# Optimization experiments

Measured on AMD Instinct MI355X. Metric: run time of the kernel, lower is better.

Reference implementation:

```python
import jax, jax.numpy as jnp
import numpy as np

NHEAD = 8
NPTS = 4
LN_EPS = 1e-5


def pos_embed(H, W, nf):
    # create_pos_embedding with normalize=True, temperature=10000, scale=2*pi
    scale = 2.0 * np.pi
    eps = 1e-6
    y_e = jnp.arange(1, H + 1, dtype=jnp.float32)
    y_e = y_e / (y_e[-1] + eps) * scale
    x_e = jnp.arange(1, W + 1, dtype=jnp.float32)
    x_e = x_e / (x_e[-1] + eps) * scale
    i = jnp.arange(nf, dtype=jnp.float32)
    dim_t = 10000.0 ** (2.0 * jnp.floor(i / 2.0) / nf)
    def enc(e):
        p = e[:, None] / dim_t  # [len, nf]
        return jnp.stack([jnp.sin(p[:, 0::2]), jnp.cos(p[:, 1::2])], axis=-1).reshape(e.shape[0], -1)
    py = enc(y_e)  # [H, nf]
    px = enc(x_e)  # [W, nf]
    pos = jnp.concatenate([
        jnp.broadcast_to(py[:, None, :], (H, W, nf)),
        jnp.broadcast_to(px[None, :, :], (H, W, nf)),
    ], axis=-1)  # [H, W, 2*nf], channel order (pos_y, pos_x) as in torch cat
    return pos.reshape(H * W, 2 * nf)


def layernorm(x, s, b):
    m = x.mean(-1, keepdims=True)
    v = x.var(-1, keepdims=True)
    return (x - m) * jax.lax.rsqrt(v + LN_EPS) * s + b


def bilinear_sample(value, loc, H, W):
    # value [B, HW, Hd, dh]; loc [B, Q, Hd, P, 2] normalized to [0,1] (x, y)
    # Matches F.grid_sample(align_corners=False, padding_mode='zeros') with grid = 2*loc - 1
    B, HW, Hd, dh = value.shape
    Q = loc.shape[1]
    v = value.transpose(0, 2, 1, 3)  # [B, Hd, HW, dh]
    x = loc[..., 0] * W - 0.5
    y = loc[..., 1] * H - 0.5
    x0 = jnp.floor(x)
    y0 = jnp.floor(y)
    wx1 = x - x0
    wy1 = y - y0
    x0i = x0.astype(jnp.int32)
    y0i = y0.astype(jnp.int32)
    def t(a):  # [B, Q, Hd, P] -> [B, Hd, Q*P]
        return a.transpose(0, 2, 1, 3).reshape(B, Hd, -1)
    def gather(xi, yi):
        valid = ((xi >= 0) & (xi < W) & (yi >= 0) & (yi < H)).astype(v.dtype)
        idx = jnp.clip(yi, 0, H - 1) * W + jnp.clip(xi, 0, W - 1)
        g = jnp.take_along_axis(v, t(idx)[..., None], axis=2)  # [B, Hd, Q*P, dh]
        return g * t(valid)[..., None]
    g00 = gather(x0i, y0i)
    g10 = gather(x0i + 1, y0i)
    g01 = gather(x0i, y0i + 1)
    g11 = gather(x0i + 1, y0i + 1)
    out = (g00 * t((1 - wx1) * (1 - wy1))[..., None]
           + g10 * t(wx1 * (1 - wy1))[..., None]
           + g01 * t((1 - wx1) * wy1)[..., None]
           + g11 * t(wx1 * wy1)[..., None])
    return out.reshape(B, Hd, Q, NPTS, dh)


def _forward(x, merge_w, merge_b, off_w, off_b, aw_w, aw_b, val_w, val_b, out_w, out_b,
             n1_s, n1_b, l1_w, l1_b, l2_w, l2_b, n2_s, n2_b, outc_w, outc_b):
    B, N, C, H, W = x.shape
    D = merge_w.shape[0]
    dh = D // NHEAD
    Q = H * W
    # merge: 1x1 conv + relu
    src = jax.nn.relu(jnp.einsum('bchw,dc->bhwd', x.reshape(B, N * C, H, W), merge_w) + merge_b)
    src = src.reshape(B, Q, D)
    pos = pos_embed(H, W, D // 2)[None].astype(x.dtype)  # [1, Q, D]
    # reference points (valid_ratios = 1): centers of cells, normalized
    ys = (jnp.arange(H, dtype=x.dtype) + 0.5) / H
    xs = (jnp.arange(W, dtype=x.dtype) + 0.5) / W
    gx, gy = jnp.meshgrid(xs, ys, indexing='xy')  # each [H, W]
    ref = jnp.stack([gx, gy], axis=-1).reshape(1, Q, 2)
    norm = jnp.array([W, H], dtype=x.dtype)  # offset normalizer (W, H) for (x, y)
    n_layers = off_w.shape[0]
    for l in range(n_layers):
        q = src + pos
        off = (q @ off_w[l] + off_b[l]).reshape(B, Q, NHEAD, NPTS, 2)
        aw = jax.nn.softmax((q @ aw_w[l] + aw_b[l]).reshape(B, Q, NHEAD, NPTS), axis=-1)
        val = (src @ val_w[l] + val_b[l]).reshape(B, Q, NHEAD, dh)
        loc = ref[:, :, None, None, :] + off / norm  # [B, Q, Hd, P, 2]
        samp = bilinear_sample(val, loc, H, W)  # [B, Hd, Q, P, dh]
        o = (samp * aw.transpose(0, 2, 1, 3)[..., None]).sum(3)  # [B, Hd, Q, dh]
        o = o.transpose(0, 2, 1, 3).reshape(B, Q, D) @ out_w[l] + out_b[l]
        src = layernorm(src + o, n1_s[l], n1_b[l])
        ff = jax.nn.relu(src @ l1_w[l] + l1_b[l]) @ l2_w[l] + l2_b[l]
        src = layernorm(src + ff, n2_s[l], n2_b[l])
    feat = src.reshape(B, H, W, D)
    out = jax.nn.relu(jnp.einsum('bhwc,dc->bhwd', feat, outc_w) + outc_b)
    return out.transpose(0, 3, 1, 2)  # [B, D, H, W]


def setup_inputs() -> dict:
    key = jax.random.key(0)
    B, N, Cb, H, W = 1, 4, 128, 120, 360
    D, Dff, L = 128, 512, 3
    ks = jax.random.split(key, 12)
    def rn(k, shape, s=0.02):
        return jax.random.normal(k, shape, dtype=jnp.float32) * s
    return {
        'x': jax.random.normal(ks[0], (B, N, Cb, H, W), dtype=jnp.float32),
        'merge_w': rn(ks[1], (D, N * Cb)),
        'merge_b': jnp.zeros((D,), jnp.float32),
        'off_w': rn(ks[2], (L, D, NHEAD * NPTS * 2)),
        'off_b': rn(ks[3], (L, NHEAD * NPTS * 2), 0.5),
        'aw_w': rn(ks[4], (L, D, NHEAD * NPTS)),
        'aw_b': jnp.zeros((L, NHEAD * NPTS), jnp.float32),
        'val_w': rn(ks[5], (L, D, D)),
        'val_b': jnp.zeros((L, D), jnp.float32),
        'out_w': rn(ks[6], (L, D, D)),
        'out_b': jnp.zeros((L, D), jnp.float32),
        'n1_s': jnp.ones((L, D), jnp.float32),
        'n1_b': jnp.zeros((L, D), jnp.float32),
        'l1_w': rn(ks[7], (L, D, Dff)),
        'l1_b': jnp.zeros((L, Dff), jnp.float32),
        'l2_w': rn(ks[8], (L, Dff, D)),
        'l2_b': jnp.zeros((L, D), jnp.float32),
        'n2_s': jnp.ones((L, D), jnp.float32),
        'n2_b': jnp.zeros((L, D), jnp.float32),
        'outc_w': rn(ks[9], (D, D)),
        'outc_b': jnp.zeros((D,), jnp.float32),
    }


def reference(x, merge_w, merge_b, off_w, off_b, aw_w, aw_b, val_w, val_b, out_w, out_b,
              n1_s, n1_b, l1_w, l1_b, l2_w, l2_b, n2_s, n2_b, outc_w, outc_b):
    return _forward(x, merge_w, merge_b, off_w, off_b, aw_w, aw_b, val_w, val_b, out_w, out_b,
                    n1_s, n1_b, l1_w, l1_b, l2_w, l2_b, n2_s, n2_b, outc_w, outc_b)
```

## Files before the change

### kernel.cpp

```cpp
#include <hip/hip_runtime.h>
#include <hip/hip_bf16.h>
#include <math.h>

#define Q_TOT 43200
#define H_ 120
#define W_ 360

typedef unsigned short ushort_t;
typedef float f32x4 __attribute__((ext_vector_type(4)));
typedef float f32x2 __attribute__((ext_vector_type(2)));
typedef unsigned short u16x4 __attribute__((ext_vector_type(4)));
typedef unsigned short u16x8 __attribute__((ext_vector_type(8)));
using short8 = __attribute__((ext_vector_type(8))) short;

static __device__ __forceinline__ float b2f(unsigned short u){
  return __uint_as_float(((unsigned)u) << 16);
}
static __device__ __forceinline__ unsigned short f2b(float f){
  unsigned u = __float_as_uint(f);
  unsigned r = (u + 0x7fffu + ((u >> 16) & 1u)) >> 16;
  return (unsigned short)r;
}

#define SWZ(row, byte) ((byte) ^ (((row) & 7) << 4))
#define SWZ3(row, byte) ((byte) ^ ((((row) ^ ((row) >> 3)) & 7) << 4))

#define CVT_TOT 615072
__global__ __launch_bounds__(256) void cvt_kernel(
    const float* p0, const float* p1, const float* p2, const float* p3,
    const float* p4, const float* p5, const float* p6, const float* p7,
    const float* p8, const float* p9, const float* p10, const float* p11,
    const float* p12, const float* p13, const float* p14, const float* p15,
    const float* p16, const float* p17, const float* p18, const float* p19,
    ushort_t* __restrict__ dst){
  const float* ps[20] = {p0,p1,p2,p3,p4,p5,p6,p7,p8,p9,p10,p11,p12,p13,p14,p15,p16,p17,p18,p19};
  const int offs[20] = {0,65536,65664,90240,90432,102720,102816,151968,152352,201504,
                        201888,202272,202656,399264,400800,597408,597792,598176,598560,614944};
  int gid = blockIdx.x*256 + threadIdx.x;
  if (gid >= CVT_TOT) return;
  int s = 0;
  #pragma unroll
  for (int i=1;i<20;i++) s += (gid >= offs[i]) ? 1 : 0;
  dst[gid] = f2b(ps[s][gid - offs[s]]);
}

#define CVTT_TOT 528384
__global__ __launch_bounds__(256) void cvtT_kernel(
    const float* __restrict__ vw, const float* __restrict__ ow,
    const float* __restrict__ w1, const float* __restrict__ w2,
    const float* __restrict__ offw, const float* __restrict__ aww,
    ushort_t* __restrict__ dst){
  int gid = blockIdx.x*256 + threadIdx.x;
  if (gid >= CVTT_TOT) return;
  if (gid >= 491520){
    int e = gid - 491520;
    int l = e / 12288, rem = e - l*12288;
    int n = rem >> 7, k = rem & 127;
    float v = (n < 64) ? offw[((size_t)l*128 + k)*64 + n]
                       : aww [((size_t)l*128 + k)*32 + (n-64)];
    dst[gid] = f2b(v);
    return;
  }
  const float* s; int K, N, off;
  if (gid < 49152)      { s = vw; K = 128; N = 128; off = 0; }
  else if (gid < 98304) { s = ow; K = 128; N = 128; off = 49152; }
  else if (gid < 294912){ s = w1; K = 128; N = 512; off = 98304; }
  else                  { s = w2; K = 512; N = 128; off = 294912; }
  int e = gid - off;
  int per = K*N;
  int l = e / per, rem = e - l*per;
  int n = rem / K, k = rem - n*K;
  dst[gid] = f2b(s[(size_t)l*per + (size_t)k*N + n]);
}

__global__ __launch_bounds__(256) void postab_kernel(float* __restrict__ tab){
  int gid = blockIdx.x*256 + threadIdx.x;
  if (gid >= 480*64) return;
  int row = gid >> 6, k = gid & 63;
  int m = k >> 1;
  float t = powf(10000.0f, (float)m * (1.0f/32.0f));
  float e;
  if (row < 120) e = (float)(row+1)   * (6.283185307179586f/((float)H_+1e-6f));
  else           e = (float)(row-119) * (6.283185307179586f/((float)W_+1e-6f));
  float p = e / t;
  tab[gid] = (k & 1) ? cosf(p) : sinf(p);
}

__global__ __launch_bounds__(256) void merge_mfma(const float* __restrict__ x,
    const ushort_t* __restrict__ mw,
    const ushort_t* __restrict__ mb,
    float* __restrict__ src){
  __shared__ ushort_t xt[2][64*128];
  const int tid = threadIdx.x;
  const int wave = tid >> 6, lane = tid & 63;
  const int lr = lane & 15, kg = lane >> 4;
  const int q0 = blockIdx.x * 64;
  const int qq4 = (tid & 15) * 4;
  const int c8  = (tid >> 4) * 8;
  const int qrow = wave*16 + lr;

  f32x4 v[8];
  #pragma unroll
  for (int cc=0;cc<8;cc++)
    v[cc] = *(const f32x4*)(x + (size_t)(c8 + cc)*Q_TOT + q0 + qq4);
  #pragma unroll
  for (int qq=0;qq<4;qq++){
    int row = qq4 + qq;
    u16x8 pk;
    #pragma unroll
    for (int cc=0;cc<8;cc++) pk[cc] = f2b(v[cc][qq]);
    *(u16x8*)((char*)xt[0] + SWZ3(row, row*256 + c8*2)) = pk;
  }
  __syncthreads();

  f32x4 acc[8];
  #pragma unroll
  for (int dt=0; dt<8; dt++) acc[dt] = (f32x4){0.f,0.f,0.f,0.f};

  for (int ch = 0; ch < 4; ch++){
    f32x4 v2[8];
    if (ch < 3){
      #pragma unroll
      for (int cc=0;cc<8;cc++)
        v2[cc] = *(const f32x4*)(x + (size_t)((ch+1)*128 + c8 + cc)*Q_TOT + q0 + qq4);
    }
    const ushort_t* xb = xt[ch & 1];
    short8 xfc[4];
    #pragma unroll
    for (int ks=0; ks<4; ks++)
      xfc[ks] = *(const short8*)((const char*)xb + SWZ3(qrow, qrow*256 + (ks*32 + kg*8)*2));
    short8 wfr[2][4];
    #pragma unroll
    for (int ks=0; ks<4; ks++)
      wfr[0][ks] = *(const short8*)(mw + (size_t)(lr)*512 + ch*128 + ks*32 + kg*8);
    #pragma unroll
    for (int dt=0; dt<8; dt++){
      if (dt < 7){
        const int nr = (dt+1)*16 + lr;
        #pragma unroll
        for (int ks=0; ks<4; ks++)
          wfr[(dt+1)&1][ks] = *(const short8*)(mw + (size_t)nr*512 + ch*128 + ks*32 + kg*8);
      }
      #pragma unroll
      for (int ks=0; ks<4; ks++)
        acc[dt] = __builtin_amdgcn_mfma_f32_16x16x32_bf16(xfc[ks], wfr[dt&1][ks], acc[dt], 0, 0, 0);
    }
    if (ch < 3){
      ushort_t* xn = xt[(ch+1) & 1];
      #pragma unroll
      for (int qq=0;qq<4;qq++){
        int row = qq4 + qq;
        u16x8 pk;
        #pragma unroll
        for (int cc=0;cc<8;cc++) pk[cc] = f2b(v2[cc][qq]);
        *(u16x8*)((char*)xn + SWZ3(row, row*256 + c8*2)) = pk;
      }
      __syncthreads();
    }
  }
  #pragma unroll
  for (int dt=0; dt<8; dt++){
    float bb = b2f(mb[dt*16 + lr]);
    #pragma unroll
    for (int r=0; r<4; r++){
      int q = q0 + wave*16 + kg*4 + r;
      float vv = acc[dt][r] + bb;
      src[(size_t)q*128 + dt*16 + lr] = vv > 0.f ? vv : 0.f;
    }
  }
}

__global__ __launch_bounds__(256) void qv_mfma(const float* __restrict__ src,
    const float* __restrict__ py, const float* __restrict__ px,
    const ushort_t* __restrict__ owt,
    const ushort_t* __restrict__ ob, const ushort_t* __restrict__ awb,
    const ushort_t* __restrict__ vwt,
    const ushort_t* __restrict__ vb,
    float* __restrict__ loc, float* __restrict__ awg,
    ushort_t* __restrict__ valbf){
  __shared__ ushort_t a_lds[64*128];
  __shared__ ushort_t qlds[64*128];
  const int tid = threadIdx.x;
  const int wave = tid >> 6, lane = tid & 63;
  const int lr = lane & 15, kg = lane >> 4;
  const int q0 = blockIdx.x * 64;
  short8 yf[2][4];
  #pragma unroll
  for (int ks=0; ks<4; ks++)
    yf[0][ks] = *(const short8*)(vwt + (size_t)lr*128 + ks*32 + kg*8);
  {
    int row = tid >> 2, c0 = (tid & 3) * 32;
    int q = q0 + row, qy = q / W_, qx = q - qy*W_;
    const float* sp = src + (size_t)q*128 + c0;
    const float* tp = (c0 < 64) ? (py + qy*64 + c0) : (px + qx*64 + (c0 - 64));
    #pragma unroll
    for (int i=0;i<4;i++){
      f32x4 s0 = *(const f32x4*)(sp + i*8), s1 = *(const f32x4*)(sp + i*8 + 4);
      f32x4 t0 = *(const f32x4*)(tp + i*8), t1 = *(const f32x4*)(tp + i*8 + 4);
      u16x8 pa, pq;
      #pragma unroll
      for (int j=0;j<4;j++){
        pa[j] = f2b(s0[j]);        pa[4+j] = f2b(s1[j]);
        pq[j] = f2b(s0[j]+t0[j]);  pq[4+j] = f2b(s1[j]+t1[j]);
      }
      int byte = row*256 + (c0 + i*8)*2;
      *(u16x8*)((char*)a_lds + SWZ(row, byte)) = pa;
      *(u16x8*)((char*)qlds + SWZ(row, byte)) = pq;
    }
  }
  __syncthreads();
  const int qrow = wave*16 + lr;
  short8 xf[4], xq[4];
  #pragma unroll
  for (int ks=0; ks<4; ks++){
    xf[ks] = *(const short8*)((const char*)a_lds + SWZ(qrow, qrow*256 + (ks*32 + kg*8)*2));
    xq[ks] = *(const short8*)((const char*)qlds + SWZ(qrow, qrow*256 + (ks*32 + kg*8)*2));
  }
  f32x4 va[8];
  #pragma unroll
  for (int dt=0; dt<8; dt++) va[dt] = (f32x4){0.f,0.f,0.f,0.f};
  #pragma unroll
  for (int dt=0; dt<8; dt++){
    if (dt < 7){
      const int nr = (dt+1)*16 + lr;
      #pragma unroll
      for (int ks=0; ks<4; ks++)
        yf[(dt+1)&1][ks] = *(const short8*)(vwt + (size_t)nr*128 + ks*32 + kg*8);
    }
    #pragma unroll
    for (int ks=0; ks<4; ks++)
      va[dt] = __builtin_amdgcn_mfma_f32_16x16x32_bf16(xf[ks], yf[dt&1][ks], va[dt], 0, 0, 0);
  }
  f32x4 qa[6];
  #pragma unroll
  for (int nt=0; nt<6; nt++) qa[nt] = (f32x4){0.f,0.f,0.f,0.f};
  short8 of[2][4];
  #pragma unroll
  for (int ks=0; ks<4; ks++)
    of[0][ks] = *(const short8*)(owt + (size_t)lr*128 + ks*32 + kg*8);
  #pragma unroll
  for (int nt=0; nt<6; nt++){
    if (nt < 5){
      const int nr = (nt+1)*16 + lr;
      #pragma unroll
      for (int ks=0; ks<4; ks++)
        of[(nt+1)&1][ks] = *(const short8*)(owt + (size_t)nr*128 + ks*32 + kg*8);
    }
    #pragma unroll
    for (int ks=0; ks<4; ks++)
      qa[nt] = __builtin_amdgcn_mfma_f32_16x16x32_bf16(xq[ks], of[nt&1][ks], qa[nt], 0, 0, 0);
  }
  #pragma unroll
  for (int dt=0; dt<8; dt++){
    float bb = b2f(vb[dt*16 + lr]);
    #pragma unroll
    for (int r=0; r<4; r++){
      int q = q0 + wave*16 + kg*4 + r;
      valbf[(size_t)q*128 + dt*16 + lr] = f2b(va[dt][r] + bb);
    }
  }
  #pragma unroll
  for (int r=0; r<4; r++){
    int q = q0 + wave*16 + kg*4 + r;
    int qy = q / W_, qx = q - qy*W_;
    float qxf = (float)qx, qyf = (float)qy;
    #pragma unroll
    for (int dt=0; dt<4; dt++){
      int n = dt*16 + lr;
      float v = qa[dt][r] + b2f(ob[n]);
      loc[(size_t)q*64 + n] = ((n & 1) ? qyf : qxf) + v;
    }
    #pragma unroll
    for (int d4=0; d4<2; d4++){
      int idx = d4*16 + lr;
      float v = qa[4+d4][r] + b2f(awb[idx]);
      float mx = fmaxf(v, __shfl_xor(v, 1, 64));
      mx = fmaxf(mx, __shfl_xor(mx, 2, 64));
      float e = expf(v - mx);
      float s = e + __shfl_xor(e, 1, 64);
      s = s + __shfl_xor(s, 2, 64);
      awg[(size_t)q*32 + idx] = e / s;
    }
  }
}

__global__ __launch_bounds__(256) void outln_mfma(const float* __restrict__ A,
    const ushort_t* __restrict__ wt,
    const ushort_t* __restrict__ bias,
    const ushort_t* __restrict__ gs, const ushort_t* __restrict__ gb,
    float* srcio){
  __shared__ ushort_t a_lds[64*128];
  const int tid = threadIdx.x;
  const int wave = tid >> 6, lane = tid & 63;
  const int lr = lane & 15, kg = lane >> 4;
  const int q0 = blockIdx.x * 64;
  short8 yf[2][4];
  #pragma unroll
  for (int ks=0; ks<4; ks++)
    yf[0][ks] = *(const short8*)(wt + (size_t)lr*128 + ks*32 + kg*8);
  {
    int row = tid >> 2, c0 = (tid & 3) * 32;
    const float* sp = A + (size_t)(q0+row)*128 + c0;
    #pragma unroll
    for (int i=0;i<4;i++){
      f32x4 v0 = *(const f32x4*)(sp + i*8);
      f32x4 v1 = *(const f32x4*)(sp + i*8 + 4);
      u16x8 pk;
      #pragma unroll
      for (int j=0;j<4;j++){ pk[j]=f2b(v0[j]); pk[4+j]=f2b(v1[j]); }
      int byte = row*256 + (c0 + i*8)*2;
      *(u16x8*)((char*)a_lds + SWZ(row, byte)) = pk;
    }
  }
  __syncthreads();
  const int qrow = wave*16 + lr;
  short8 xf[4];
  #pragma unroll
  for (int ks=0; ks<4; ks++)
    xf[ks] = *(const short8*)((const char*)a_lds + SWZ(qrow, qrow*256 + (ks*32 + kg*8)*2));
  f32x4 acc[8];
  #pragma unroll
  for (int dt=0; dt<8; dt++) acc[dt] = (f32x4){0.f,0.f,0.f,0.f};
  #pragma unroll
  for (int dt=0; dt<8; dt++){
    if (dt < 7){
      const int nr = (dt+1)*16 + lr;
      #pragma unroll
      for (int ks=0; ks<4; ks++)
        yf[(dt+1)&1][ks] = *(const short8*)(wt + (size_t)nr*128 + ks*32 + kg*8);
    }
    #pragma unroll
    for (int ks=0; ks<4; ks++)
      acc[dt] = __builtin_amdgcn_mfma_f32_16x16x32_bf16(xf[ks], yf[dt&1][ks], acc[dt], 0, 0, 0);
  }
  float g4[8], be4[8], bi4[8];
  #pragma unroll
  for (int dt=0; dt<8; dt++){
    g4[dt] = b2f(gs[dt*16+lr]); be4[dt] = b2f(gb[dt*16+lr]); bi4[dt] = b2f(bias[dt*16+lr]);
  }
  #pragma unroll
  for (int r=0; r<4; r++){
    const int q = q0 + wave*16 + kg*4 + r;
    float vals[8];
    float s1 = 0.f, s2 = 0.f;
    #pragma unroll
    for (int dt=0; dt<8; dt++){
      float v = acc[dt][r] + bi4[dt] + srcio[(size_t)q*128 + dt*16 + lr];
      vals[dt] = v; s1 += v; s2 += v*v;
    }
    #pragma unroll
    for (int m=1; m<16; m<<=1){ s1 += __shfl_xor(s1, m, 64); s2 += __shfl_xor(s2, m, 64); }
    float mean = s1*(1.f/128.f);
    float var  = s2*(1.f/128.f) - mean*mean;
    float inv  = rsqrtf(var + 1e-5f);
    #pragma unroll
    for (int dt=0; dt<8; dt++)
      srcio[(size_t)q*128 + dt*16 + lr] = (vals[dt]-mean)*inv*g4[dt] + be4[dt];
  }
}

__global__ __launch_bounds__(512, 4) void ffn_mfma(
    const ushort_t* __restrict__ w1t,
    const ushort_t* __restrict__ b1,
    const ushort_t* __restrict__ w2t,
    const ushort_t* __restrict__ b2,
    const ushort_t* __restrict__ gs, const ushort_t* __restrict__ gb,
    float* srcio){
  __shared__ char smem[49152];
  ushort_t* a_lds = (ushort_t*)smem;
  ushort_t* h_lds = (ushort_t*)(smem + 16384);
  float* scr = (float*)smem;
  const int tid = threadIdx.x;
  const int wave = tid >> 6, lane = tid & 63;
  const int lr = lane & 15, kg = lane >> 4;
  const int q0 = blockIdx.x * 64;
  {
    int row = tid >> 3, c0 = (tid & 7) * 16;
    const float* sp = srcio + (size_t)(q0+row)*128 + c0;
    #pragma unroll
    for (int i=0;i<2;i++){
      f32x4 v0 = *(const f32x4*)(sp + i*8);
      f32x4 v1 = *(const f32x4*)(sp + i*8 + 4);
      u16x8 pk;
      #pragma unroll
      for (int j=0;j<4;j++){ pk[j]=f2b(v0[j]); pk[4+j]=f2b(v1[j]); }
      int byte = row*256 + (c0 + i*8)*2;
      *(u16x8*)((char*)a_lds + SWZ(row, byte)) = pk;
    }
  }
  const int drow = wave*16 + lr;
  f32x4 accd[4];
  #pragma unroll
  for (int qt=0; qt<4; qt++) accd[qt] = (f32x4){0.f,0.f,0.f,0.f};
  __syncthreads();
  for (int half=0; half<2; half++){
    short8 wf[2][4];
    #pragma unroll
    for (int nt=0; nt<2; nt++){
      const int nrow = (half*16 + wave*2 + nt)*16 + lr;
      #pragma unroll
      for (int ks=0; ks<4; ks++)
        wf[nt][ks] = *(const short8*)(w1t + (size_t)nrow*128 + ks*32 + kg*8);
    }
    short8 yg[8];
    #pragma unroll
    for (int ks=0; ks<8; ks++)
      yg[ks] = *(const short8*)(w2t + (size_t)drow*512 + half*256 + ks*32 + kg*8);
    #pragma unroll
    for (int nt=0; nt<2; nt++){
      const int ngt = half*16 + wave*2 + nt;
      u16x4 bb = *(const u16x4*)(b1 + ngt*16 + kg*4);
      float bf[4];
      #pragma unroll
      for (int j=0;j<4;j++) bf[j] = b2f(bb[j]);
      #pragma unroll
      for (int qt=0; qt<4; qt++){
        f32x4 acc = (f32x4){0.f,0.f,0.f,0.f};
        const int q = qt*16 + lr;
        #pragma unroll
        for (int ks=0; ks<4; ks++){
          short8 yf = *(const short8*)((const char*)a_lds + SWZ(q, q*256 + (ks*32 + kg*8)*2));
          acc = __builtin_amdgcn_mfma_f32_16x16x32_bf16(wf[nt][ks], yf, acc, 0, 0, 0);
        }
        const int nl = (ngt & 15)*16 + kg*4;
        u16x4 hp;
        #pragma unroll
        for (int r=0;r<4;r++){ float v = acc[r] + bf[r]; hp[r] = f2b(v > 0.f ? v : 0.f); }
        *(u16x4*)((char*)h_lds + SWZ(q, q*512 + nl*2)) = hp;
      }
    }
    __syncthreads();
    #pragma unroll
    for (int qt=0; qt<4; qt++){
      const int qrow = qt*16 + lr;
      short8 xh[8];
      #pragma unroll
      for (int ks=0; ks<8; ks++)
        xh[ks] = *(const short8*)((const char*)h_lds + SWZ(qrow, qrow*512 + (ks*32 + kg*8)*2));
      #pragma unroll
      for (int ks=0; ks<8; ks++)
        accd[qt] = __builtin_amdgcn_mfma_f32_16x16x32_bf16(xh[ks], yg[ks], accd[qt], 0, 0, 0);
    }
    __syncthreads();
  }
  #pragma unroll
  for (int qt=0; qt<4; qt++)
    #pragma unroll
    for (int r=0; r<4; r++)
      scr[(qt*16 + kg*4 + r)*132 + wave*16 + lr] = accd[qt][r];
  __syncthreads();
  {
    const int c = lane*2;
    float bi0 = b2f(b2[c]),  bi1 = b2f(b2[c+1]);
    float g0  = b2f(gs[c]),  g1  = b2f(gs[c+1]);
    float be0 = b2f(gb[c]),  be1 = b2f(gb[c+1]);
    #pragma unroll
    for (int i=0; i<8; i++){
      const int ql = wave*8 + i;
      const size_t qg = (size_t)(q0 + ql)*128 + c;
      f32x2 res = *(const f32x2*)&srcio[qg];
      float v0 = scr[ql*132 + c]     + bi0 + res[0];
      float v1 = scr[ql*132 + c + 1] + bi1 + res[1];
      float s1 = v0 + v1, s2 = v0*v0 + v1*v1;
      #pragma unroll
      for (int m=1; m<64; m<<=1){ s1 += __shfl_xor(s1, m, 64); s2 += __shfl_xor(s2, m, 64); }
      float mean = s1*(1.f/128.f);
      float var  = s2*(1.f/128.f) - mean*mean;
      float inv  = rsqrtf(var + 1e-5f);
      f32x2 outv;
      outv[0] = (v0-mean)*inv*g0 + be0;
      outv[1] = (v1-mean)*inv*g1 + be1;
      *(f32x2*)&srcio[qg] = outv;
    }
  }
}

__global__ __launch_bounds__(256) void sample_kernel(const ushort_t* __restrict__ val,
    const float* __restrict__ loc, const float* __restrict__ awg,
    float* __restrict__ o){
  __shared__ float sl[4][64];
  __shared__ float sa[4][32];
  const int tid = threadIdx.x;
  const int q0 = blockIdx.x * 4;
  sl[0][tid & 255] = loc[(size_t)q0*64 + tid];
  if (tid < 128) sa[0][tid] = awg[(size_t)q0*32 + tid];
  __syncthreads();
  const int ql = tid >> 6, cp = (tid & 63) * 2;
  const int h = cp >> 4;
  float a0 = 0.f, a1 = 0.f;
  #pragma unroll
  for (int p=0;p<4;p++){
    float x = sl[ql][h*8 + p*2];
    float y = sl[ql][h*8 + p*2 + 1];
    float wgt = sa[ql][h*4 + p];
    float x0f = floorf(x), y0f = floorf(y);
    float wx = x - x0f, wy = y - y0f;
    int ix = (int)x0f, iy = (int)y0f;
    int x0c = min(max(ix, 0), W_-1),   x1c = min(max(ix+1, 0), W_-1);
    int y0c = min(max(iy, 0), H_-1),   y1c = min(max(iy+1, 0), H_-1);
    float vx0 = (ix   >= 0 && ix   < W_) ? 1.f : 0.f;
    float vx1 = (ix+1 >= 0 && ix+1 < W_) ? 1.f : 0.f;
    float vy0 = (iy   >= 0 && iy   < H_) ? 1.f : 0.f;
    float vy1 = (iy+1 >= 0 && iy+1 < H_) ? 1.f : 0.f;
    float w00 = (1.f-wx)*(1.f-wy)*vx0*vy0 * wgt;
    float w10 = wx*(1.f-wy)*vx1*vy0 * wgt;
    float w01 = (1.f-wx)*wy*vx0*vy1 * wgt;
    float w11 = wx*wy*vx1*vy1 * wgt;
    unsigned g00 = *(const unsigned*)(val + (size_t)(y0c*W_ + x0c)*128 + cp);
    unsigned g10 = *(const unsigned*)(val + (size_t)(y0c*W_ + x1c)*128 + cp);
    unsigned g01 = *(const unsigned*)(val + (size_t)(y1c*W_ + x0c)*128 + cp);
    unsigned g11 = *(const unsigned*)(val + (size_t)(y1c*W_ + x1c)*128 + cp);
    a0 += w00*b2f((ushort_t)g00) + w10*b2f((ushort_t)g10)
        + w01*b2f((ushort_t)g01) + w11*b2f((ushort_t)g11);
    a1 += w00*b2f((ushort_t)(g00>>16)) + w10*b2f((ushort_t)(g10>>16))
        + w01*b2f((ushort_t)(g01>>16)) + w11*b2f((ushort_t)(g11>>16));
  }
  f32x2 r; r[0] = a0; r[1] = a1;
  *(f32x2*)&o[(size_t)(q0+ql)*128 + cp] = r;
}

__global__ __launch_bounds__(256) void outc_mfma(const float* __restrict__ A,
    const ushort_t* __restrict__ wt,
    const ushort_t* __restrict__ bias,
    float* __restrict__ outp){
  __shared__ ushort_t a_lds[64*128];
  const int tid = threadIdx.x;
  const int wave = tid >> 6, lane = tid & 63;
  const int lr = lane & 15, kg = lane >> 4;
  const int q0 = blockIdx.x * 64;
  short8 yf[2][4];
  #pragma unroll
  for (int ks=0; ks<4; ks++)
    yf[0][ks] = *(const short8*)(wt + (size_t)lr*128 + ks*32 + kg*8);
  {
    int row = tid >> 2, c0 = (tid & 3) * 32;
    const float* sp = A + (size_t)(q0+row)*128 + c0;
    #pragma unroll
    for (int i=0;i<4;i++){
      f32x4 v0 = *(const f32x4*)(sp + i*8);
      f32x4 v1 = *(const f32x4*)(sp + i*8 + 4);
      u16x8 pk;
      #pragma unroll
      for (int j=0;j<4;j++){ pk[j]=f2b(v0[j]); pk[4+j]=f2b(v1[j]); }
      int byte = row*256 + (c0 + i*8)*2;
      *(u16x8*)((char*)a_lds + SWZ(row, byte)) = pk;
    }
  }
  __syncthreads();
  const int qrow = wave*16 + lr;
  short8 xf[4];
  #pragma unroll
  for (int ks=0; ks<4; ks++)
    xf[ks] = *(const short8*)((const char*)a_lds + SWZ(qrow, qrow*256 + (ks*32 + kg*8)*2));
  f32x4 acc[8];
  #pragma unroll
  for (int dt=0; dt<8; dt++) acc[dt] = (f32x4){0.f,0.f,0.f,0.f};
  #pragma unroll
  for (int dt=0; dt<8; dt++){
    if (dt < 7){
      const int nr = (dt+1)*16 + lr;
      #pragma unroll
      for (int ks=0; ks<4; ks++)
        yf[(dt+1)&1][ks] = *(const short8*)(wt + (size_t)nr*128 + ks*32 + kg*8);
    }
    #pragma unroll
    for (int ks=0; ks<4; ks++)
      acc[dt] = __builtin_amdgcn_mfma_f32_16x16x32_bf16(xf[ks], yf[dt&1][ks], acc[dt], 0, 0, 0);
  }
  #pragma unroll
  for (int dt=0; dt<8; dt++){
    float bb = b2f(bias[dt*16 + lr]);
    #pragma unroll
    for (int r=0; r<4; r++){
      int q = q0 + wave*16 + kg*4 + r;
      float v = acc[dt][r] + bb;
      v = v > 0.f ? v : 0.f;
      outp[(size_t)(dt*16 + lr)*Q_TOT + q] = v;
    }
  }
}

extern "C" void kernel_launch(void* const* d_in, const int* in_sizes, int n_in,
                              void* d_out, int out_size, void* d_ws, size_t ws_size,
                              hipStream_t stream){
  const float* x = (const float*)d_in[0];

  float* src = (float*)d_ws;
  float* loc = src + (size_t)Q_TOT*128;
  float* aw  = loc + (size_t)Q_TOT*64;
  float* o   = aw  + (size_t)Q_TOT*32;
  ushort_t* valbf = (ushort_t*)(o + (size_t)Q_TOT*128);
  ushort_t* wbf   = valbf + (size_t)Q_TOT*128;
  ushort_t* tbase = wbf + 615072;
  float* postab = (float*)(tbase + 528384);
  float* pytab = postab;
  float* pxtab = postab + 120*64;

  const ushort_t* mw     = wbf + 0;
  const ushort_t* mb     = wbf + 65536;
  const ushort_t* off_b  = wbf + 90240;
  const ushort_t* aw_b   = wbf + 102720;
  const ushort_t* val_b  = wbf + 151968;
  const ushort_t* out_b  = wbf + 201504;
  const ushort_t* n1_s   = wbf + 201888;
  const ushort_t* n1_b   = wbf + 202272;
  const ushort_t* l1_b   = wbf + 399264;
  const ushort_t* l2_b   = wbf + 597408;
  const ushort_t* n2_s   = wbf + 597792;
  const ushort_t* n2_b   = wbf + 598176;
  const ushort_t* outc_w = wbf + 598560;
  const ushort_t* outc_b = wbf + 614944;
  const ushort_t* val_wt = tbase + 0;
  const ushort_t* out_wt = tbase + 49152;
  const ushort_t* l1_wt  = tbase + 98304;
  const ushort_t* l2_wt  = tbase + 294912;
  const ushort_t* oaw_t  = tbase + 491520;

  cvt_kernel<<<(CVT_TOT+255)/256, 256, 0, stream>>>(
      (const float*)d_in[1],  (const float*)d_in[2],  (const float*)d_in[3],
      (const float*)d_in[4],  (const float*)d_in[5],  (const float*)d_in[6],
      (const float*)d_in[7],  (const float*)d_in[8],  (const float*)d_in[9],
      (const float*)d_in[10], (const float*)d_in[11], (const float*)d_in[12],
      (const float*)d_in[13], (const float*)d_in[14], (const float*)d_in[15],
      (const float*)d_in[16], (const float*)d_in[17], (const float*)d_in[18],
      (const float*)d_in[19], (const float*)d_in[20], wbf);
  cvtT_kernel<<<CVTT_TOT/256, 256, 0, stream>>>(
      (const float*)d_in[7], (const float*)d_in[9],
      (const float*)d_in[13], (const float*)d_in[15],
      (const float*)d_in[3], (const float*)d_in[5], tbase);
  postab_kernel<<<120, 256, 0, stream>>>(postab);

  merge_mfma<<<Q_TOT/64, 256, 0, stream>>>(x, mw, mb, src);
  for (int l = 0; l < 3; l++){
    qv_mfma<<<Q_TOT/64, 256, 0, stream>>>(src, pytab, pxtab,
        oaw_t + (size_t)l*96*128, off_b + (size_t)l*64, aw_b + (size_t)l*32,
        val_wt + (size_t)l*128*128, val_b + (size_t)l*128,
        loc, aw, valbf);
    sample_kernel<<<Q_TOT/4, 256, 0, stream>>>(valbf, loc, aw, o);
    outln_mfma<<<Q_TOT/64, 256, 0, stream>>>(o,
        out_wt + (size_t)l*128*128, out_b + (size_t)l*128,
        n1_s + (size_t)l*128, n1_b + (size_t)l*128, src);
    ffn_mfma<<<Q_TOT/64, 512, 0, stream>>>(
        l1_wt + (size_t)l*512*128, l1_b + (size_t)l*512,
        l2_wt + (size_t)l*128*512, l2_b + (size_t)l*128,
        n2_s + (size_t)l*128, n2_b + (size_t)l*128, src);
  }
  outc_mfma<<<Q_TOT/64, 256, 0, stream>>>(src, outc_w, outc_b, (float*)d_out);
}
```

Baseline: 416.3 us.

## Store activations in bf16 and halve per-block query tiles across GEMM kernels

The residual stream (src) and the sampled attention output are now stored in bf16 rather than fp32. This halves global memory traffic between kernels and removes the per-kernel fp32-to-bf16 conversion on load. In addition, the qv, outln, ffn and outc kernels process 32 queries per block instead of 64, with waves split across output columns, to raise block count and occupancy. The risk is extra rounding error, because the residual and LayerNorm outputs are kept in bf16 between layers.

Measured after the change: 448.5 us. +7.8%, slower.

```diff
diff --git a/kernel.cpp b/kernel.cpp
--- a/kernel.cpp
+++ b/kernel.cpp
@@ -8,7 +8,6 @@
 
 typedef unsigned short ushort_t;
 typedef float f32x4 __attribute__((ext_vector_type(4)));
-typedef float f32x2 __attribute__((ext_vector_type(2)));
 typedef unsigned short u16x4 __attribute__((ext_vector_type(4)));
 typedef unsigned short u16x8 __attribute__((ext_vector_type(8)));
 using short8 = __attribute__((ext_vector_type(8))) short;
@@ -86,10 +85,10 @@
   tab[gid] = (k & 1) ? cosf(p) : sinf(p);
 }
 
-__global__ __launch_bounds__(256) void merge_mfma(const float* __restrict__ x,
+__global__ __launch_bounds__(256, 3) void merge_mfma(const float* __restrict__ x,
     const ushort_t* __restrict__ mw,
     const ushort_t* __restrict__ mb,
-    float* __restrict__ src){
+    ushort_t* __restrict__ srcbf){
   __shared__ ushort_t xt[2][64*128];
   const int tid = threadIdx.x;
   const int wave = tid >> 6, lane = tid & 63;
@@ -165,12 +164,12 @@
     for (int r=0; r<4; r++){
       int q = q0 + wave*16 + kg*4 + r;
       float vv = acc[dt][r] + bb;
-      src[(size_t)q*128 + dt*16 + lr] = vv > 0.f ? vv : 0.f;
-    }
-  }
-}
-
-__global__ __launch_bounds__(256) void qv_mfma(const float* __restrict__ src,
+      srcbf[(size_t)q*128 + dt*16 + lr] = f2b(vv > 0.f ? vv : 0.f);
+    }
+  }
+}
+
+__global__ __launch_bounds__(256, 3) void qv_mfma(const ushort_t* __restrict__ srcbf,
     const float* __restrict__ py, const float* __restrict__ px,
     const ushort_t* __restrict__ owt,
     const ushort_t* __restrict__ ob, const ushort_t* __restrict__ awb,
@@ -178,220 +177,223 @@
     const ushort_t* __restrict__ vb,
     float* __restrict__ loc, float* __restrict__ awg,
     ushort_t* __restrict__ valbf){
-  __shared__ ushort_t a_lds[64*128];
-  __shared__ ushort_t qlds[64*128];
+  __shared__ ushort_t a_lds[32*128];
+  __shared__ ushort_t qlds[32*128];
   const int tid = threadIdx.x;
   const int wave = tid >> 6, lane = tid & 63;
   const int lr = lane & 15, kg = lane >> 4;
-  const int q0 = blockIdx.x * 64;
+  const int q0 = blockIdx.x * 32;
+  const int qh = wave >> 1, role = wave & 1;
+  #pragma unroll
+  for (int i=0;i<2;i++){
+    int idx = i*256 + tid;
+    int row = idx >> 4, ch = idx & 15;
+    int q = q0 + row, qy = q / W_, qx = q - qy*W_;
+    u16x8 s = *(const u16x8*)(srcbf + (size_t)q*128 + ch*8);
+    int c0 = ch*8;
+    const float* tp = (c0 < 64) ? (py + qy*64 + c0) : (px + qx*64 + (c0-64));
+    f32x4 t0 = *(const f32x4*)tp, t1 = *(const f32x4*)(tp+4);
+    u16x8 pq;
+    #pragma unroll
+    for (int j=0;j<4;j++){
+      pq[j]   = f2b(b2f(s[j])   + t0[j]);
+      pq[4+j] = f2b(b2f(s[4+j]) + t1[j]);
+    }
+    int byte = row*256 + c0*2;
+    *(u16x8*)((char*)a_lds + SWZ(row, byte)) = s;
+    *(u16x8*)((char*)qlds + SWZ(row, byte)) = pq;
+  }
+  __syncthreads();
+  const int qrow = qh*16 + lr;
+  short8 xf[4], xq[4];
+  #pragma unroll
+  for (int ks=0; ks<4; ks++){
+    xf[ks] = *(const short8*)((const char*)a_lds + SWZ(qrow, qrow*256 + (ks*32+kg*8)*2));
+    xq[ks] = *(const short8*)((const char*)qlds + SWZ(qrow, qrow*256 + (ks*32+kg*8)*2));
+  }
+  const int dtb = role*4, ntb = role*3;
+  f32x4 va[4];
+  #pragma unroll
+  for (int i=0;i<4;i++) va[i] = (f32x4){0.f,0.f,0.f,0.f};
   short8 yf[2][4];
   #pragma unroll
   for (int ks=0; ks<4; ks++)
-    yf[0][ks] = *(const short8*)(vwt + (size_t)lr*128 + ks*32 + kg*8);
-  {
-    int row = tid >> 2, c0 = (tid & 3) * 32;
-    int q = q0 + row, qy = q / W_, qx = q - qy*W_;
-    const float* sp = src + (size_t)q*128 + c0;
-    const float* tp = (c0 < 64) ? (py + qy*64 + c0) : (px + qx*64 + (c0 - 64));
-    #pragma unroll
-    for (int i=0;i<4;i++){
-      f32x4 s0 = *(const f32x4*)(sp + i*8), s1 = *(const f32x4*)(sp + i*8 + 4);
-      f32x4 t0 = *(const f32x4*)(tp + i*8), t1 = *(const f32x4*)(tp + i*8 + 4);
-      u16x8 pa, pq;
-      #pragma unroll
-      for (int j=0;j<4;j++){
-        pa[j] = f2b(s0[j]);        pa[4+j] = f2b(s1[j]);
-        pq[j] = f2b(s0[j]+t0[j]);  pq[4+j] = f2b(s1[j]+t1[j]);
-      }
-      int byte = row*256 + (c0 + i*8)*2;
-      *(u16x8*)((char*)a_lds + SWZ(row, byte)) = pa;
-      *(u16x8*)((char*)qlds + SWZ(row, byte)) = pq;
-    }
-  }
-  __syncthreads();
-  const int qrow = wave*16 + lr;
-  short8 xf[4], xq[4];
-  #pragma unroll
-  for (int ks=0; ks<4; ks++){
-    xf[ks] = *(const short8*)((const char*)a_lds + SWZ(qrow, qrow*256 + (ks*32 + kg*8)*2));
-    xq[ks] = *(const short8*)((const char*)qlds + SWZ(qrow, qrow*256 + (ks*32 + kg*8)*2));
-  }
-  f32x4 va[8];
-  #pragma unroll
-  for (int dt=0; dt<8; dt++) va[dt] = (f32x4){0.f,0.f,0.f,0.f};
-  #pragma unroll
-  for (int dt=0; dt<8; dt++){
-    if (dt < 7){
-      const int nr = (dt+1)*16 + lr;
+    yf[0][ks] = *(const short8*)(vwt + (size_t)(dtb*16+lr)*128 + ks*32 + kg*8);
+  #pragma unroll
+  for (int dtl=0; dtl<4; dtl++){
+    if (dtl < 3){
+      const int nr = (dtb+dtl+1)*16 + lr;
       #pragma unroll
       for (int ks=0; ks<4; ks++)
-        yf[(dt+1)&1][ks] = *(const short8*)(vwt + (size_t)nr*128 + ks*32 + kg*8);
+        yf[(dtl+1)&1][ks] = *(const short8*)(vwt + (size_t)nr*128 + ks*32 + kg*8);
     }
     #pragma unroll
     for (int ks=0; ks<4; ks++)
-      va[dt] = __builtin_amdgcn_mfma_f32_16x16x32_bf16(xf[ks], yf[dt&1][ks], va[dt], 0, 0, 0);
-  }
-  f32x4 qa[6];
-  #pragma unroll
-  for (int nt=0; nt<6; nt++) qa[nt] = (f32x4){0.f,0.f,0.f,0.f};
+      va[dtl] = __builtin_amdgcn_mfma_f32_16x16x32_bf16(xf[ks], yf[dtl&1][ks], va[dtl], 0, 0, 0);
+  }
+  f32x4 qa[3];
+  #pragma unroll
+  for (int i=0;i<3;i++) qa[i] = (f32x4){0.f,0.f,0.f,0.f};
   short8 of[2][4];
   #pragma unroll
   for (int ks=0; ks<4; ks++)
-    of[0][ks] = *(const short8*)(owt + (size_t)lr*128 + ks*32 + kg*8);
-  #pragma unroll
-  for (int nt=0; nt<6; nt++){
-    if (nt < 5){
-      const int nr = (nt+1)*16 + lr;
+    of[0][ks] = *(const short8*)(owt + (size_t)(ntb*16+lr)*128 + ks*32 + kg*8);
+  #pragma unroll
+  for (int ntl=0; ntl<3; ntl++){
+    if (ntl < 2){
+      const int nr = (ntb+ntl+1)*16 + lr;
       #pragma unroll
       for (int ks=0; ks<4; ks++)
-        of[(nt+1)&1][ks] = *(const short8*)(owt + (size_t)nr*128 + ks*32 + kg*8);
+        of[(ntl+1)&1][ks] = *(const short8*)(owt + (size_t)nr*128 + ks*32 + kg*8);
     }
     #pragma unroll
     for (int ks=0; ks<4; ks++)
-      qa[nt] = __builtin_amdgcn_mfma_f32_16x16x32_bf16(xq[ks], of[nt&1][ks], qa[nt], 0, 0, 0);
-  }
-  #pragma unroll
-  for (int dt=0; dt<8; dt++){
+      qa[ntl] = __builtin_amdgcn_mfma_f32_16x16x32_bf16(xq[ks], of[ntl&1][ks], qa[ntl], 0, 0, 0);
+  }
+  #pragma unroll
+  for (int dtl=0; dtl<4; dtl++){
+    int dt = dtb + dtl;
     float bb = b2f(vb[dt*16 + lr]);
     #pragma unroll
     for (int r=0; r<4; r++){
-      int q = q0 + wave*16 + kg*4 + r;
-      valbf[(size_t)q*128 + dt*16 + lr] = f2b(va[dt][r] + bb);
+      int q = q0 + qh*16 + kg*4 + r;
+      valbf[(size_t)q*128 + dt*16 + lr] = f2b(va[dtl][r] + bb);
     }
   }
   #pragma unroll
   for (int r=0; r<4; r++){
-    int q = q0 + wave*16 + kg*4 + r;
+    int q = q0 + qh*16 + kg*4 + r;
     int qy = q / W_, qx = q - qy*W_;
     float qxf = (float)qx, qyf = (float)qy;
-    #pragma unroll
-    for (int dt=0; dt<4; dt++){
-      int n = dt*16 + lr;
-      float v = qa[dt][r] + b2f(ob[n]);
-      loc[(size_t)q*64 + n] = ((n & 1) ? qyf : qxf) + v;
-    }
-    #pragma unroll
-    for (int d4=0; d4<2; d4++){
-      int idx = d4*16 + lr;
-      float v = qa[4+d4][r] + b2f(awb[idx]);
-      float mx = fmaxf(v, __shfl_xor(v, 1, 64));
-      mx = fmaxf(mx, __shfl_xor(mx, 2, 64));
-      float e = expf(v - mx);
-      float s = e + __shfl_xor(e, 1, 64);
-      s = s + __shfl_xor(s, 2, 64);
-      awg[(size_t)q*32 + idx] = e / s;
-    }
-  }
-}
-
-__global__ __launch_bounds__(256) void outln_mfma(const float* __restrict__ A,
+    if (role == 0){
+      #pragma unroll
+      for (int ntl=0; ntl<3; ntl++){
+        int n = ntl*16 + lr;
+        float v = qa[ntl][r] + b2f(ob[n]);
+        loc[(size_t)q*64 + n] = ((n & 1) ? qyf : qxf) + v;
+      }
+    } else {
+      {
+        int n = 48 + lr;
+        float v = qa[0][r] + b2f(ob[n]);
+        loc[(size_t)q*64 + n] = ((n & 1) ? qyf : qxf) + v;
+      }
+      #pragma unroll
+      for (int d4=0; d4<2; d4++){
+        int idx = d4*16 + lr;
+        float v = qa[1+d4][r] + b2f(awb[idx]);
+        float mx = fmaxf(v, __shfl_xor(v, 1, 64));
+        mx = fmaxf(mx, __shfl_xor(mx, 2, 64));
+        float e = expf(v - mx);
+        float s = e + __shfl_xor(e, 1, 64);
+        s = s + __shfl_xor(s, 2, 64);
+        awg[(size_t)q*32 + idx] = e / s;
+      }
+    }
+  }
+}
+
+__global__ __launch_bounds__(256, 3) void outln_mfma(const ushort_t* __restrict__ obf,
     const ushort_t* __restrict__ wt,
     const ushort_t* __restrict__ bias,
     const ushort_t* __restrict__ gs, const ushort_t* __restrict__ gb,
-    float* srcio){
-  __shared__ ushort_t a_lds[64*128];
+    ushort_t* srcbf){
+  __shared__ char smem[16896];
+  ushort_t* a_lds = (ushort_t*)smem;
+  float* scr = (float*)smem;
   const int tid = threadIdx.x;
   const int wave = tid >> 6, lane = tid & 63;
   const int lr = lane & 15, kg = lane >> 4;
-  const int q0 = blockIdx.x * 64;
+  const int q0 = blockIdx.x * 32;
+  const int qh = wave >> 1, nh = wave & 1;
+  #pragma unroll
+  for (int i=0;i<2;i++){
+    int idx = i*256 + tid;
+    int row = idx >> 4, ch = idx & 15;
+    u16x8 s = *(const u16x8*)(obf + (size_t)(q0+row)*128 + ch*8);
+    *(u16x8*)((char*)a_lds + SWZ(row, row*256 + ch*16)) = s;
+  }
+  __syncthreads();
+  const int qrow = qh*16 + lr;
+  short8 xf[4];
+  #pragma unroll
+  for (int ks=0; ks<4; ks++)
+    xf[ks] = *(const short8*)((const char*)a_lds + SWZ(qrow, qrow*256 + (ks*32+kg*8)*2));
+  __syncthreads();
+  f32x4 acc[4];
+  #pragma unroll
+  for (int i=0;i<4;i++) acc[i] = (f32x4){0.f,0.f,0.f,0.f};
   short8 yf[2][4];
   #pragma unroll
   for (int ks=0; ks<4; ks++)
-    yf[0][ks] = *(const short8*)(wt + (size_t)lr*128 + ks*32 + kg*8);
+    yf[0][ks] = *(const short8*)(wt + (size_t)((nh*4)*16+lr)*128 + ks*32 + kg*8);
+  #pragma unroll
+  for (int dtl=0; dtl<4; dtl++){
+    if (dtl < 3){
+      const int nr = (nh*4+dtl+1)*16 + lr;
+      #pragma unroll
+      for (int ks=0; ks<4; ks++)
+        yf[(dtl+1)&1][ks] = *(const short8*)(wt + (size_t)nr*128 + ks*32 + kg*8);
+    }
+    #pragma unroll
+    for (int ks=0; ks<4; ks++)
+      acc[dtl] = __builtin_amdgcn_mfma_f32_16x16x32_bf16(xf[ks], yf[dtl&1][ks], acc[dtl], 0, 0, 0);
+  }
+  #pragma unroll
+  for (int dtl=0; dtl<4; dtl++)
+    #pragma unroll
+    for (int r=0; r<4; r++)
+      scr[(qh*16 + kg*4 + r)*132 + nh*64 + dtl*16 + lr] = acc[dtl][r];
+  __syncthreads();
   {
-    int row = tid >> 2, c0 = (tid & 3) * 32;
-    const float* sp = A + (size_t)(q0+row)*128 + c0;
-    #pragma unroll
-    for (int i=0;i<4;i++){
-      f32x4 v0 = *(const f32x4*)(sp + i*8);
-      f32x4 v1 = *(const f32x4*)(sp + i*8 + 4);
-      u16x8 pk;
-      #pragma unroll
-      for (int j=0;j<4;j++){ pk[j]=f2b(v0[j]); pk[4+j]=f2b(v1[j]); }
-      int byte = row*256 + (c0 + i*8)*2;
-      *(u16x8*)((char*)a_lds + SWZ(row, byte)) = pk;
-    }
-  }
-  __syncthreads();
-  const int qrow = wave*16 + lr;
-  short8 xf[4];
-  #pragma unroll
-  for (int ks=0; ks<4; ks++)
-    xf[ks] = *(const short8*)((const char*)a_lds + SWZ(qrow, qrow*256 + (ks*32 + kg*8)*2));
-  f32x4 acc[8];
-  #pragma unroll
-  for (int dt=0; dt<8; dt++) acc[dt] = (f32x4){0.f,0.f,0.f,0.f};
-  #pragma unroll
-  for (int dt=0; dt<8; dt++){
-    if (dt < 7){
-      const int nr = (dt+1)*16 + lr;
-      #pragma unroll
-      for (int ks=0; ks<4; ks++)
-        yf[(dt+1)&1][ks] = *(const short8*)(wt + (size_t)nr*128 + ks*32 + kg*8);
-    }
-    #pragma unroll
-    for (int ks=0; ks<4; ks++)
-      acc[dt] = __builtin_amdgcn_mfma_f32_16x16x32_bf16(xf[ks], yf[dt&1][ks], acc[dt], 0, 0, 0);
-  }
-  float g4[8], be4[8], bi4[8];
-  #pragma unroll
-  for (int dt=0; dt<8; dt++){
-    g4[dt] = b2f(gs[dt*16+lr]); be4[dt] = b2f(gb[dt*16+lr]); bi4[dt] = b2f(bias[dt*16+lr]);
-  }
-  #pragma unroll
-  for (int r=0; r<4; r++){
-    const int q = q0 + wave*16 + kg*4 + r;
-    float vals[8];
-    float s1 = 0.f, s2 = 0.f;
-    #pragma unroll
-    for (int dt=0; dt<8; dt++){
-      float v = acc[dt][r] + bi4[dt] + srcio[(size_t)q*128 + dt*16 + lr];
-      vals[dt] = v; s1 += v; s2 += v*v;
-    }
-    #pragma unroll
-    for (int m=1; m<16; m<<=1){ s1 += __shfl_xor(s1, m, 64); s2 += __shfl_xor(s2, m, 64); }
-    float mean = s1*(1.f/128.f);
-    float var  = s2*(1.f/128.f) - mean*mean;
-    float inv  = rsqrtf(var + 1e-5f);
-    #pragma unroll
-    for (int dt=0; dt<8; dt++)
-      srcio[(size_t)q*128 + dt*16 + lr] = (vals[dt]-mean)*inv*g4[dt] + be4[dt];
-  }
-}
-
-__global__ __launch_bounds__(512, 4) void ffn_mfma(
+    const int c = lane*2;
+    float bi0 = b2f(bias[c]), bi1 = b2f(bias[c+1]);
+    float g0  = b2f(gs[c]),   g1  = b2f(gs[c+1]);
+    float be0 = b2f(gb[c]),   be1 = b2f(gb[c+1]);
+    #pragma unroll
+    for (int i=0; i<8; i++){
+      int ql = wave*8 + i;
+      unsigned rr = *(const unsigned*)(srcbf + (size_t)(q0+ql)*128 + c);
+      float v0 = scr[ql*132 + c]     + bi0 + b2f((ushort_t)rr);
+      float v1 = scr[ql*132 + c + 1] + bi1 + b2f((ushort_t)(rr >> 16));
+      float s1 = v0 + v1, s2 = v0*v0 + v1*v1;
+      #pragma unroll
+      for (int m=1; m<64; m<<=1){ s1 += __shfl_xor(s1, m, 64); s2 += __shfl_xor(s2, m, 64); }
+      float mean = s1*(1.f/128.f);
+      float var  = s2*(1.f/128.f) - mean*mean;
+      float inv  = rsqrtf(var + 1e-5f);
+      float o0 = (v0-mean)*inv*g0 + be0;
+      float o1 = (v1-mean)*inv*g1 + be1;
+      unsigned pk = (unsigned)f2b(o0) | ((unsigned)f2b(o1) << 16);
+      *(unsigned*)(srcbf + (size_t)(q0+ql)*128 + c) = pk;
+    }
+  }
+}
+
+__global__ __launch_bounds__(512, 2) void ffn_mfma(
     const ushort_t* __restrict__ w1t,
     const ushort_t* __restrict__ b1,
     const ushort_t* __restrict__ w2t,
     const ushort_t* __restrict__ b2,
     const ushort_t* __restrict__ gs, const ushort_t* __restrict__ gb,
-    float* srcio){
-  __shared__ char smem[49152];
+    ushort_t* srcbf){
+  __shared__ char smem[24576];
   ushort_t* a_lds = (ushort_t*)smem;
-  ushort_t* h_lds = (ushort_t*)(smem + 16384);
+  ushort_t* h_lds = (ushort_t*)(smem + 8192);
   float* scr = (float*)smem;
   const int tid = threadIdx.x;
   const int wave = tid >> 6, lane = tid & 63;
   const int lr = lane & 15, kg = lane >> 4;
-  const int q0 = blockIdx.x * 64;
+  const int q0 = blockIdx.x * 32;
   {
-    int row = tid >> 3, c0 = (tid & 7) * 16;
-    const float* sp = srcio + (size_t)(q0+row)*128 + c0;
-    #pragma unroll
-    for (int i=0;i<2;i++){
-      f32x4 v0 = *(const f32x4*)(sp + i*8);
-      f32x4 v1 = *(const f32x4*)(sp + i*8 + 4);
-      u16x8 pk;
-      #pragma unroll
-      for (int j=0;j<4;j++){ pk[j]=f2b(v0[j]); pk[4+j]=f2b(v1[j]); }
-      int byte = row*256 + (c0 + i*8)*2;
-      *(u16x8*)((char*)a_lds + SWZ(row, byte)) = pk;
-    }
+    int row = tid >> 4, ch = tid & 15;
+    u16x8 s = *(const u16x8*)(srcbf + (size_t)(q0+row)*128 + ch*8);
+    *(u16x8*)((char*)a_lds + SWZ(row, row*256 + ch*16)) = s;
   }
   const int drow = wave*16 + lr;
-  f32x4 accd[4];
-  #pragma unroll
-  for (int qt=0; qt<4; qt++) accd[qt] = (f32x4){0.f,0.f,0.f,0.f};
+  f32x4 accd[2];
+  accd[0] = (f32x4){0.f,0.f,0.f,0.f};
+  accd[1] = (f32x4){0.f,0.f,0.f,0.f};
   __syncthreads();
   for (int half=0; half<2; half++){
     short8 wf[2][4];
@@ -414,7 +416,7 @@
       #pragma unroll
       for (int j=0;j<4;j++) bf[j] = b2f(bb[j]);
       #pragma unroll
-      for (int qt=0; qt<4; qt++){
+      for (int qt=0; qt<2; qt++){
         f32x4 acc = (f32x4){0.f,0.f,0.f,0.f};
         const int q = qt*16 + lr;
         #pragma unroll
@@ -431,7 +433,7 @@
     }
     __syncthreads();
     #pragma unroll
-    for (int qt=0; qt<4; qt++){
+    for (int qt=0; qt<2; qt++){
       const int qrow = qt*16 + lr;
       short8 xh[8];
       #pragma unroll
@@ -444,40 +446,39 @@
     __syncthreads();
   }
   #pragma unroll
-  for (int qt=0; qt<4; qt++)
+  for (int qt=0; qt<2; qt++)
     #pragma unroll
     for (int r=0; r<4; r++)
       scr[(qt*16 + kg*4 + r)*132 + wave*16 + lr] = accd[qt][r];
   __syncthreads();
   {
     const int c = lane*2;
-    float bi0 = b2f(b2[c]),  bi1 = b2f(b2[c+1]);
-    float g0  = b2f(gs[c]),  g1  = b2f(gs[c+1]);
-    float be0 = b2f(gb[c]),  be1 = b2f(gb[c+1]);
-    #pragma unroll
-    for (int i=0; i<8; i++){
-      const int ql = wave*8 + i;
-      const size_t qg = (size_t)(q0 + ql)*128 + c;
-      f32x2 res = *(const f32x2*)&srcio[qg];
-      float v0 = scr[ql*132 + c]     + bi0 + res[0];
-      float v1 = scr[ql*132 + c + 1] + bi1 + res[1];
+    float bi0 = b2f(b2[c]), bi1 = b2f(b2[c+1]);
+    float g0  = b2f(gs[c]), g1  = b2f(gs[c+1]);
+    float be0 = b2f(gb[c]), be1 = b2f(gb[c+1]);
+    #pragma unroll
+    for (int i=0; i<4; i++){
+      int ql = wave*4 + i;
+      unsigned rr = *(const unsigned*)(srcbf + (size_t)(q0+ql)*128 + c);
+      float v0 = scr[ql*132 + c]     + bi0 + b2f((ushort_t)rr);
+      float v1 = scr[ql*132 + c + 1] + bi1 + b2f((ushort_t)(rr >> 16));
       float s1 = v0 + v1, s2 = v0*v0 + v1*v1;
       #pragma unroll
       for (int m=1; m<64; m<<=1){ s1 += __shfl_xor(s1, m, 64); s2 += __shfl_xor(s2, m, 64); }
       float mean = s1*(1.f/128.f);
       float var  = s2*(1.f/128.f) - mean*mean;
       float inv  = rsqrtf(var + 1e-5f);
-      f32x2 outv;
-      outv[0] = (v0-mean)*inv*g0 + be0;
-      outv[1] = (v1-mean)*inv*g1 + be1;
-      *(f32x2*)&srcio[qg] = outv;
+      float o0 = (v0-mean)*inv*g0 + be0;
+      float o1 = (v1-mean)*inv*g1 + be1;
+      unsigned pk = (unsigned)f2b(o0) | ((unsigned)f2b(o1) << 16);
+      *(unsigned*)(srcbf + (size_t)(q0+ql)*128 + c) = pk;
     }
   }
 }
 
 __global__ __launch_bounds__(256) void sample_kernel(const ushort_t* __restrict__ val,
     const float* __restrict__ loc, const float* __restrict__ awg,
-    float* __restrict__ o){
+    ushort_t* __restrict__ obf){
   __shared__ float sl[4][64];
   __shared__ float sa[4][32];
   const int tid = threadIdx.x;
@@ -515,67 +516,62 @@
     a1 += w00*b2f((ushort_t)(g00>>16)) + w10*b2f((ushort_t)(g10>>16))
         + w01*b2f((ushort_t)(g01>>16)) + w11*b2f((ushort_t)(g11>>16));
   }
-  f32x2 r; r[0] = a0; r[1] = a1;
-  *(f32x2*)&o[(size_t)(q0+ql)*128 + cp] = r;
-}
-
-__global__ __launch_bounds__(256) void outc_mfma(const float* __restrict__ A,
+  unsigned pk = (unsigned)f2b(a0) | ((unsigned)f2b(a1) << 16);
+  *(unsigned*)&obf[(size_t)(q0+ql)*128 + cp] = pk;
+}
+
+__global__ __launch_bounds__(256, 3) void outc_mfma(const ushort_t* __restrict__ srcbf,
     const ushort_t* __restrict__ wt,
     const ushort_t* __restrict__ bias,
     float* __restrict__ outp){
-  __shared__ ushort_t a_lds[64*128];
+  __shared__ ushort_t a_lds[32*128];
   const int tid = threadIdx.x;
   const int wave = tid >> 6, lane = tid & 63;
   const int lr = lane & 15, kg = lane >> 4;
-  const int q0 = blockIdx.x * 64;
+  const int q0 = blockIdx.x * 32;
+  const int qh = wave >> 1, nh = wave & 1;
+  #pragma unroll
+  for (int i=0;i<2;i++){
+    int idx = i*256 + tid;
+    int row = idx >> 4, ch = idx & 15;
+    u16x8 s = *(const u16x8*)(srcbf + (size_t)(q0+row)*128 + ch*8);
+    *(u16x8*)((char*)a_lds + SWZ(row, row*256 + ch*16)) = s;
+  }
+  __syncthreads();
+  const int qrow = qh*16 + lr;
+  short8 xf[4];
+  #pragma unroll
+  for (int ks=0; ks<4; ks++)
+    xf[ks] = *(const short8*)((const char*)a_lds + SWZ(qrow, qrow*256 + (ks*32+kg*8)*2));
+  f32x4 acc[4];
+  #pragma unroll
+  for (int i=0;i<4;i++) acc[i] = (f32x4){0.f,0.f,0.f,0.f};
   short8 yf[2][4];
   #pragma unroll
   for (int ks=0; ks<4; ks++)
-    yf[0][ks] = *(const short8*)(wt + (size_t)lr*128 + ks*32 + kg*8);
-  {
-    int row = tid >> 2, c0 = (tid & 3) * 32;
-    const float* sp = A + (size_t)(q0+row)*128 + c0;
-    #pragma unroll
-    for (int i=0;i<4;i++){
-      f32x4 v0 = *(const f32x4*)(sp + i*8);
-      f32x4 v1 = *(const f32x4*)(sp + i*8 + 4);
-      u16x8 pk;
-      #pragma unroll
-      for (int j=0;j<4;j++){ pk[j]=f2b(v0[j]); pk[4+j]=f2b(v1[j]); }
-      int byte = row*256 + (c0 + i*8)*2;
-      *(u16x8*)((char*)a_lds + SWZ(row, byte)) = pk;
-    }
-  }
-  __syncthreads();
-  const int qrow = wave*16 + lr;
-  short8 xf[4];
-  #pragma unroll
-  for (int ks=0; ks<4; ks++)
-    xf[ks] = *(const short8*)((const char*)a_lds + SWZ(qrow, qrow*256 + (ks*32 + kg*8)*2));
-  f32x4 acc[8];
-  #pragma unroll
-  for (int dt=0; dt<8; dt++) acc[dt] = (f32x4){0.f,0.f,0.f,0.f};
-  #pragma unroll
-  for (int dt=0; dt<8; dt++){
-    if (dt < 7){
-      const int nr = (dt+1)*16 + lr;
+    yf[0][ks] = *(const short8*)(wt + (size_t)((nh*4)*16+lr)*128 + ks*32 + kg*8);
+  #pragma unroll
+  for (int dtl=0; dtl<4; dtl++){
+    if (dtl < 3){
+      const int nr = (nh*4+dtl+1)*16 + lr;
       #pragma unroll
       for (int ks=0; ks<4; ks++)
-        yf[(dt+1)&1][ks] = *(const short8*)(wt + (size_t)nr*128 + ks*32 + kg*8);
+        yf[(dtl+1)&1][ks] = *(const short8*)(wt + (size_t)nr*128 + ks*32 + kg*8);
     }
     #pragma unroll
     for (int ks=0; ks<4; ks++)
-      acc[dt] = __builtin_amdgcn_mfma_f32_16x16x32_bf16(xf[ks], yf[dt&1][ks], acc[dt], 0, 0, 0);
-  }
-  #pragma unroll
-  for (int dt=0; dt<8; dt++){
-    float bb = b2f(bias[dt*16 + lr]);
+      acc[dtl] = __builtin_amdgcn_mfma_f32_16x16x32_bf16(xf[ks], yf[dtl&1][ks], acc[dtl], 0, 0, 0);
+  }
+  #pragma unroll
+  for (int dtl=0; dtl<4; dtl++){
+    int d = (nh*4+dtl)*16 + lr;
+    float bb = b2f(bias[d]);
     #pragma unroll
     for (int r=0; r<4; r++){
-      int q = q0 + wave*16 + kg*4 + r;
-      float v = acc[dt][r] + bb;
+      int q = q0 + qh*16 + kg*4 + r;
+      float v = acc[dtl][r] + bb;
       v = v > 0.f ? v : 0.f;
-      outp[(size_t)(dt*16 + lr)*Q_TOT + q] = v;
+      outp[(size_t)d*Q_TOT + q] = v;
     }
   }
 }
@@ -585,12 +581,12 @@
                               hipStream_t stream){
   const float* x = (const float*)d_in[0];
 
-  float* src = (float*)d_ws;
-  float* loc = src + (size_t)Q_TOT*128;
+  ushort_t* srcbf = (ushort_t*)d_ws;
+  ushort_t* obf   = srcbf + (size_t)Q_TOT*128;
+  ushort_t* valbf = obf   + (size_t)Q_TOT*128;
+  float* loc = (float*)(valbf + (size_t)Q_TOT*128);
   float* aw  = loc + (size_t)Q_TOT*64;
-  float* o   = aw  + (size_t)Q_TOT*32;
-  ushort_t* valbf = (ushort_t*)(o + (size_t)Q_TOT*128);
-  ushort_t* wbf   = valbf + (size_t)Q_TOT*128;
+  ushort_t* wbf   = (ushort_t*)(aw + (size_t)Q_TOT*32);
   ushort_t* tbase = wbf + 615072;
   float* postab = (float*)(tbase + 528384);
   float* pytab = postab;
@@ -630,20 +626,20 @@
       (const float*)d_in[3], (const float*)d_in[5], tbase);
   postab_kernel<<<120, 256, 0, stream>>>(postab);
 
-  merge_mfma<<<Q_TOT/64, 256, 0, stream>>>(x, mw, mb, src);
+  merge_mfma<<<Q_TOT/64, 256, 0, stream>>>(x, mw, mb, srcbf);
   for (int l = 0; l < 3; l++){
-    qv_mfma<<<Q_TOT/64, 256, 0, stream>>>(src, pytab, pxtab,
+    qv_mfma<<<Q_TOT/32, 256, 0, stream>>>(srcbf, pytab, pxtab,
         oaw_t + (size_t)l*96*128, off_b + (size_t)l*64, aw_b + (size_t)l*32,
         val_wt + (size_t)l*128*128, val_b + (size_t)l*128,
         loc, aw, valbf);
-    sample_kernel<<<Q_TOT/4, 256, 0, stream>>>(valbf, loc, aw, o);
-    outln_mfma<<<Q_TOT/64, 256, 0, stream>>>(o,
+    sample_kernel<<<Q_TOT/4, 256, 0, stream>>>(valbf, loc, aw, obf);
+    outln_mfma<<<Q_TOT/32, 256, 0, stream>>>(obf,
         out_wt + (size_t)l*128*128, out_b + (size_t)l*128,
-        n1_s + (size_t)l*128, n1_b + (size_t)l*128, src);
-    ffn_mfma<<<Q_TOT/64, 512, 0, stream>>>(
+        n1_s + (size_t)l*128, n1_b + (size_t)l*128, srcbf);
+    ffn_mfma<<<Q_TOT/32, 512, 0, stream>>>(
         l1_wt + (size_t)l*512*128, l1_b + (size_t)l*512,
         l2_wt + (size_t)l*128*512, l2_b + (size_t)l*128,
-        n2_s + (size_t)l*128, n2_b + (size_t)l*128, src);
-  }
-  outc_mfma<<<Q_TOT/64, 256, 0, stream>>>(src, outc_w, outc_b, (float*)d_out);
-}
+        n2_s + (size_t)l*128, n2_b + (size_t)l*128, srcbf);
+  }
+  outc_mfma<<<Q_TOT/32, 256, 0, stream>>>(srcbf, outc_w, outc_b, (float*)d_out);
+}
```
